# Optimization experiments

Hardware: AMD Instinct MI355X
Metric: run time of the kernel (lower is better)

## Reference

```python
import jax, jax.numpy as jnp
import numpy as np

N_NODES = 100000
N_EDGES = 6400000
F_IN = 128
F_OUT = 16


def setup_inputs() -> dict:
    key = jax.random.key(0)
    k1, k2, k3 = jax.random.split(key, 3)
    x = jax.random.normal(k1, (N_NODES, F_IN), dtype=jnp.float32)
    edge_index = jax.random.randint(k2, (2, N_EDGES), 0, N_NODES, dtype=jnp.int64)
    W = jax.random.normal(k3, (F_IN, F_OUT), dtype=jnp.float32) / np.sqrt(F_IN)
    b = jnp.zeros((F_OUT,), dtype=jnp.float32)
    return {"x": x, "edge_index": edge_index, "W": W, "b": b}


def reference(x, edge_index, W, b):
    # GCNConv (PyG defaults: add self-loops, symmetric normalization) -> tanh -> mean pool
    N = x.shape[0]
    loops = jnp.arange(N, dtype=edge_index.dtype)
    row = jnp.concatenate([edge_index[0], loops])  # source nodes
    col = jnp.concatenate([edge_index[1], loops])  # target nodes
    # degree of target nodes (edge weight 1.0)
    deg = jax.ops.segment_sum(jnp.ones(row.shape[0], dtype=x.dtype), col, num_segments=N)
    dinv = jnp.where(deg > 0, jax.lax.rsqrt(deg), 0.0)
    norm = dinv[row] * dinv[col]  # [E+N]
    h = x @ W  # [N, F_OUT] transform first (cheaper than transforming messages)
    msgs = h[row] * norm[:, None]  # gather + scale
    out = jax.ops.segment_sum(msgs, col, num_segments=N) + b  # scatter-add
    h = jnp.tanh(out)
    # MeanAggregation over all nodes -> single graph embedding [1, F_OUT]
    return jnp.mean(h, axis=0, keepdims=True)
```

## Files before the change

kernel.cpp:

```cpp
#include <hip/hip_runtime.h>
#include <math.h>

#define N_NODES 100000
#define N_EDGES 6400000
#define F_IN 128
#define F_OUT 16
#define NB 391
#define NBLK 1000
#define EPB 6400
#define BCAP 20480
#define KPB 5
#define QSCALE 1024.0f
#define QINV   (1.0f / 1024.0f)
#define FIN_GRID 640
#define GN 128
#define GSTRIDE 132

__global__ void __launch_bounds__(256) place_kernel(const int* __restrict__ row,
        const int* __restrict__ col, int* __restrict__ cur,
        unsigned int* __restrict__ packed) {
    __shared__ int hist[NB];
    __shared__ int scanb[512];
    __shared__ int base[NB];
    __shared__ int gadj[NB];
    __shared__ unsigned int tile[EPB];
    __shared__ unsigned char tileb8[EPB];
    const int t = threadIdx.x, k = blockIdx.x;
    const int e0 = k * EPB;
    for (int i = t; i < NB; i += 256) hist[i] = 0;
    __syncthreads();
    for (int i = t; i < EPB; i += 256)
        atomicAdd(&hist[col[e0 + i] >> 8], 1);
    __syncthreads();
    scanb[t] = (t < NB) ? hist[t] : 0;
    scanb[t + 256] = (t + 256 < NB) ? hist[t + 256] : 0;
    __syncthreads();
    for (int off = 1; off < 512; off <<= 1) {
        int a  = (t >= off) ? scanb[t - off] : 0;
        int a2 = scanb[t + 256 - off];
        __syncthreads();
        scanb[t] += a; scanb[t + 256] += a2;
        __syncthreads();
    }
    if (t < NB) base[t] = scanb[t] - hist[t];
    if (t + 256 < NB) base[t + 256] = scanb[t + 256] - hist[t + 256];
    __syncthreads();
    const int b256 = base[256];
    for (int bb = t; bb < NB; bb += 256) {
        int c = hist[bb];
        int g = (c > 0) ? atomicAdd(&cur[bb], c) : 0;
        gadj[bb] = bb * BCAP + g - base[bb];
        hist[bb] = 0;
    }
    __syncthreads();
    for (int i = t; i < EPB; i += 256) {
        int c = col[e0 + i];
        int r = row[e0 + i];
        int bb = c >> 8;
        int pos = base[bb] + atomicAdd(&hist[bb], 1);
        tile[pos] = ((unsigned)r << 8) | (unsigned)(c & 255);
        tileb8[pos] = (unsigned char)bb;
    }
    __syncthreads();
    for (int i = t; i < EPB; i += 256) {
        int bb = (int)tileb8[i] + ((i >= b256) ? 256 : 0);
        packed[gadj[bb] + i] = tile[i];
    }
}

__global__ void __launch_bounds__(256) deg_kernel(const unsigned int* __restrict__ packed,
        const int* __restrict__ cur, int* __restrict__ deg) {
    __shared__ int dh[256];
    const int t = threadIdx.x;
    dh[t] = 0;
    __syncthreads();
    const int b = blockIdx.x, part = blockIdx.y;
    const int cnt = cur[b];
    const int s = b * BCAP;
    const int chunk = (cnt + 3) >> 2;
    const int cs = s + part * chunk;
    const int ce = s + min((part + 1) * chunk, cnt);
    for (int i = cs + t; i < ce; i += 256)
        atomicAdd(&dh[packed[i] & 255u], 1);
    __syncthreads();
    const int node = (b << 8) + t;
    if (node < N_NODES && dh[t]) atomicAdd(&deg[node], dh[t]);
}

__global__ void __launch_bounds__(256) gemm_kernel(const float* __restrict__ x,
        const float* __restrict__ W, const int* __restrict__ deg,
        short* __restrict__ gq, int* __restrict__ acc) {
    __shared__ float Ws[F_IN * F_OUT];
    __shared__ float xs[GN * GSTRIDE];
    const int t = threadIdx.x;
    const int n0 = blockIdx.x * GN;
    {
        const size_t z0 = (size_t)blockIdx.x * 2048;
        for (int j = t; j < 2048; j += 256) {
            size_t idx = z0 + j;
            if (idx < (size_t)N_NODES * F_OUT) acc[idx] = 0;
        }
    }
    const float4* W4 = (const float4*)W;
    for (int i = t; i < 512; i += 256) ((float4*)Ws)[i] = W4[i];
    for (int i = t; i < GN * 32; i += 256) {
        int r = i >> 5, c4 = i & 31;
        float4 v = make_float4(0.f, 0.f, 0.f, 0.f);
        if (n0 + r < N_NODES)
            v = ((const float4*)(x + (size_t)(n0 + r) * F_IN))[c4];
        *(float4*)(xs + r * GSTRIDE + c4 * 4) = v;
    }
    __syncthreads();
    const int fq = t & 3, n2 = t >> 2;
    const float* xrA = xs + n2 * GSTRIDE;
    const float* xrB = xs + (n2 + 64) * GSTRIDE;
    float accA[4] = {0.f, 0.f, 0.f, 0.f};
    float accB[4] = {0.f, 0.f, 0.f, 0.f};
    #pragma unroll 8
    for (int kq = 0; kq < 32; kq++) {
        float4 xa = *(const float4*)(xrA + kq * 4);
        float4 xb = *(const float4*)(xrB + kq * 4);
        #pragma unroll
        for (int j = 0; j < 4; j++) {
            float4 w = *(const float4*)(Ws + (kq * 4 + j) * 16 + fq * 4);
            float a = (j == 0) ? xa.x : (j == 1) ? xa.y : (j == 2) ? xa.z : xa.w;
            float bv = (j == 0) ? xb.x : (j == 1) ? xb.y : (j == 2) ? xb.z : xb.w;
            accA[0] += a * w.x;  accA[1] += a * w.y;
            accA[2] += a * w.z;  accA[3] += a * w.w;
            accB[0] += bv * w.x; accB[1] += bv * w.y;
            accB[2] += bv * w.z; accB[3] += bv * w.w;
        }
    }
    const int gA = n0 + n2, gB = n0 + n2 + 64;
    if (gA < N_NODES) {
        float dinv = rsqrtf((float)deg[gA] + 1.0f);
        short4 o;
        float v0 = fminf(fmaxf(accA[0] * dinv * QSCALE, -32000.f), 32000.f);
        float v1 = fminf(fmaxf(accA[1] * dinv * QSCALE, -32000.f), 32000.f);
        float v2 = fminf(fmaxf(accA[2] * dinv * QSCALE, -32000.f), 32000.f);
        float v3 = fminf(fmaxf(accA[3] * dinv * QSCALE, -32000.f), 32000.f);
        o.x = (short)__float2int_rn(v0); o.y = (short)__float2int_rn(v1);
        o.z = (short)__float2int_rn(v2); o.w = (short)__float2int_rn(v3);
        *(short4*)(gq + (size_t)gA * 16 + fq * 4) = o;
    }
    if (gB < N_NODES) {
        float dinv = rsqrtf((float)deg[gB] + 1.0f);
        short4 o;
        float v0 = fminf(fmaxf(accB[0] * dinv * QSCALE, -32000.f), 32000.f);
        float v1 = fminf(fmaxf(accB[1] * dinv * QSCALE, -32000.f), 32000.f);
        float v2 = fminf(fmaxf(accB[2] * dinv * QSCALE, -32000.f), 32000.f);
        float v3 = fminf(fmaxf(accB[3] * dinv * QSCALE, -32000.f), 32000.f);
        o.x = (short)__float2int_rn(v0); o.y = (short)__float2int_rn(v1);
        o.z = (short)__float2int_rn(v2); o.w = (short)__float2int_rn(v3);
        *(short4*)(gq + (size_t)gB * 16 + fq * 4) = o;
    }
}

__global__ void __launch_bounds__(256) scatter_kernel(
        const unsigned int* __restrict__ packed, const int* __restrict__ cur,
        const short* __restrict__ gq, int* __restrict__ acc) {
    __shared__ int sacc[256 * F_OUT];
    const int t = threadIdx.x;
    for (int i = t; i < 256 * F_OUT; i += 256) sacc[i] = 0;
    __syncthreads();
    const int b = blockIdx.x, part = blockIdx.y;
    const int cnt = cur[b];
    const int s = b * BCAP;
    const int chunk = (cnt + KPB - 1) / KPB;
    const int cs = s + part * chunk;
    const int ce = s + min((part + 1) * chunk, cnt);
    const int f = t & 15, eg = t >> 4;
    int i = cs + eg;
    for (; i + 48 < ce; i += 64) {
        unsigned p0 = packed[i];
        unsigned p1 = packed[i + 16];
        unsigned p2 = packed[i + 32];
        unsigned p3 = packed[i + 48];
        int v0 = gq[(p0 >> 8) * 16 + f];
        int v1 = gq[(p1 >> 8) * 16 + f];
        int v2 = gq[(p2 >> 8) * 16 + f];
        int v3 = gq[(p3 >> 8) * 16 + f];
        atomicAdd(&sacc[((p0 & 255u) << 4) + f], v0);
        atomicAdd(&sacc[((p1 & 255u) << 4) + f], v1);
        atomicAdd(&sacc[((p2 & 255u) << 4) + f], v2);
        atomicAdd(&sacc[((p3 & 255u) << 4) + f], v3);
    }
    for (; i < ce; i += 16) {
        unsigned p0 = packed[i];
        atomicAdd(&sacc[((p0 & 255u) << 4) + f], (int)gq[(p0 >> 8) * 16 + f]);
    }
    __syncthreads();
    const int nbase = b << 8;
    for (int j = t; j < 256 * F_OUT; j += 256) {
        int v = sacc[j];
        if (v && nbase + (j >> 4) < N_NODES)
            atomicAdd(&acc[((size_t)nbase << 4) + j], v);
    }
}

__global__ void __launch_bounds__(256) finalize_kernel(const int* __restrict__ acc,
        const short* __restrict__ gq, const int* __restrict__ deg,
        const float* __restrict__ b, double* __restrict__ dsum,
        int* __restrict__ done, float* __restrict__ out) {
    __shared__ float s[4][16];
    __shared__ int lastflag;
    const int tid = threadIdx.x;
    const int f = tid & 15;
    const float bf = b[f];
    float local = 0.f;
    for (int i = blockIdx.x * blockDim.x + tid; i < N_NODES * F_OUT;
         i += gridDim.x * blockDim.x) {
        const int n = i >> 4;
        int ai = acc[i] + (int)gq[i];
        float dinvn = rsqrtf((float)deg[n] + 1.0f);
        local += tanhf(dinvn * ((float)ai * QINV) + bf);
    }
    local += __shfl_down(local, 32);
    local += __shfl_down(local, 16);
    const int lane = tid & 63, wave = tid >> 6;
    if (lane < 16) s[wave][lane] = local;
    __syncthreads();
    if (tid < 16) {
        float v = s[0][tid] + s[1][tid] + s[2][tid] + s[3][tid];
        atomicAdd(&dsum[tid], (double)v);
    }
    if (tid == 0) {
        __threadfence();
        lastflag = (atomicAdd(done, 1) == (int)gridDim.x - 1);
    }
    __syncthreads();
    if (lastflag && tid < 16) {
        double v = atomicAdd(&dsum[tid], 0.0);
        out[tid] = (float)(v * (1.0 / (double)N_NODES));
    }
}

extern "C" void kernel_launch(void* const* d_in, const int* in_sizes, int n_in,
                              void* d_out, int out_size, void* d_ws, size_t ws_size,
                              hipStream_t stream) {
    const float* x  = (const float*)d_in[0];
    const int*   ei = (const int*)d_in[1];
    const float* W  = (const float*)d_in[2];
    const float* b  = (const float*)d_in[3];
    float* out = (float*)d_out;

    const int* row = ei;
    const int* col = ei + N_EDGES;

    char* p = (char*)d_ws;
    double*       dsum   = (double*)p;        p += 128;
    int*          done   = (int*)p;           p += 32;
    int*          cur    = (int*)p;           p += 1600;
    int*          deg    = (int*)p;           p += (size_t)N_NODES * 4;
    int*          acc    = (int*)p;           p += (size_t)N_NODES * F_OUT * 4;
    short*        gq     = (short*)p;         p += (size_t)N_NODES * F_OUT * 2;
    unsigned int* packed = (unsigned int*)p;

    hipMemsetAsync(dsum, 0, 128 + 32 + 1600 + (size_t)N_NODES * 4, stream);

    place_kernel   <<<NBLK, 256, 0, stream>>>(row, col, cur, packed);
    deg_kernel     <<<dim3(NB, 4), 256, 0, stream>>>(packed, cur, deg);
    gemm_kernel    <<<(N_NODES + GN - 1) / GN, 256, 0, stream>>>(x, W, deg, gq, acc);
    scatter_kernel <<<dim3(NB, KPB), 256, 0, stream>>>(packed, cur, gq, acc);
    finalize_kernel<<<FIN_GRID, 256, 0, stream>>>(acc, gq, deg, b, dsum, done, out);
}
```

Before: 292.7 us.

## Fuse finalize into scatter via last-block-per-bucket, simplify GEMM to direct loads

Removes the separate finalize kernel. The last of the KPB scatter blocks for each 256-node bucket, detected with a per-bucket counter, computes tanh and the partial mean for that bucket, and a grid-level counter writes the output. The GEMM drops its shared-memory staging of x and reads rows straight from global memory, 64 nodes per block. KPB rises from 5 to 8 for more scatter parallelism. This saves a launch and a full pass over acc, at the cost of extra atomics and fences in the scatter tail.

```diff
diff --git a/kernel.cpp b/kernel.cpp
--- a/kernel.cpp
+++ b/kernel.cpp
@@ -9,12 +9,9 @@
 #define NBLK 1000
 #define EPB 6400
 #define BCAP 20480
-#define KPB 5
+#define KPB 8
 #define QSCALE 1024.0f
 #define QINV   (1.0f / 1024.0f)
-#define FIN_GRID 640
-#define GN 128
-#define GSTRIDE 132
 
 __global__ void __launch_bounds__(256) place_kernel(const int* __restrict__ row,
         const int* __restrict__ col, int* __restrict__ cur,
@@ -91,84 +88,64 @@
         const float* __restrict__ W, const int* __restrict__ deg,
         short* __restrict__ gq, int* __restrict__ acc) {
     __shared__ float Ws[F_IN * F_OUT];
-    __shared__ float xs[GN * GSTRIDE];
     const int t = threadIdx.x;
-    const int n0 = blockIdx.x * GN;
     {
-        const size_t z0 = (size_t)blockIdx.x * 2048;
-        for (int j = t; j < 2048; j += 256) {
+        const size_t z0 = (size_t)blockIdx.x * 1024;
+        for (int j = t; j < 1024; j += 256) {
             size_t idx = z0 + j;
             if (idx < (size_t)N_NODES * F_OUT) acc[idx] = 0;
         }
     }
     const float4* W4 = (const float4*)W;
     for (int i = t; i < 512; i += 256) ((float4*)Ws)[i] = W4[i];
-    for (int i = t; i < GN * 32; i += 256) {
-        int r = i >> 5, c4 = i & 31;
-        float4 v = make_float4(0.f, 0.f, 0.f, 0.f);
-        if (n0 + r < N_NODES)
-            v = ((const float4*)(x + (size_t)(n0 + r) * F_IN))[c4];
-        *(float4*)(xs + r * GSTRIDE + c4 * 4) = v;
-    }
-    __syncthreads();
-    const int fq = t & 3, n2 = t >> 2;
-    const float* xrA = xs + n2 * GSTRIDE;
-    const float* xrB = xs + (n2 + 64) * GSTRIDE;
-    float accA[4] = {0.f, 0.f, 0.f, 0.f};
-    float accB[4] = {0.f, 0.f, 0.f, 0.f};
-    #pragma unroll 8
+    __syncthreads();
+    const int fq = t & 3, n = t >> 2;
+    const int node = blockIdx.x * 64 + n;
+    if (node >= N_NODES) return;
+    const float4* xr = (const float4*)(x + (size_t)node * F_IN);
+    float a0 = 0.f, a1 = 0.f, a2 = 0.f, a3 = 0.f;
+    #pragma unroll 4
     for (int kq = 0; kq < 32; kq++) {
-        float4 xa = *(const float4*)(xrA + kq * 4);
-        float4 xb = *(const float4*)(xrB + kq * 4);
-        #pragma unroll
-        for (int j = 0; j < 4; j++) {
-            float4 w = *(const float4*)(Ws + (kq * 4 + j) * 16 + fq * 4);
-            float a = (j == 0) ? xa.x : (j == 1) ? xa.y : (j == 2) ? xa.z : xa.w;
-            float bv = (j == 0) ? xb.x : (j == 1) ? xb.y : (j == 2) ? xb.z : xb.w;
-            accA[0] += a * w.x;  accA[1] += a * w.y;
-            accA[2] += a * w.z;  accA[3] += a * w.w;
-            accB[0] += bv * w.x; accB[1] += bv * w.y;
-            accB[2] += bv * w.z; accB[3] += bv * w.w;
-        }
-    }
-    const int gA = n0 + n2, gB = n0 + n2 + 64;
-    if (gA < N_NODES) {
-        float dinv = rsqrtf((float)deg[gA] + 1.0f);
-        short4 o;
-        float v0 = fminf(fmaxf(accA[0] * dinv * QSCALE, -32000.f), 32000.f);
-        float v1 = fminf(fmaxf(accA[1] * dinv * QSCALE, -32000.f), 32000.f);
-        float v2 = fminf(fmaxf(accA[2] * dinv * QSCALE, -32000.f), 32000.f);
-        float v3 = fminf(fmaxf(accA[3] * dinv * QSCALE, -32000.f), 32000.f);
-        o.x = (short)__float2int_rn(v0); o.y = (short)__float2int_rn(v1);
-        o.z = (short)__float2int_rn(v2); o.w = (short)__float2int_rn(v3);
-        *(short4*)(gq + (size_t)gA * 16 + fq * 4) = o;
-    }
-    if (gB < N_NODES) {
-        float dinv = rsqrtf((float)deg[gB] + 1.0f);
-        short4 o;
-        float v0 = fminf(fmaxf(accB[0] * dinv * QSCALE, -32000.f), 32000.f);
-        float v1 = fminf(fmaxf(accB[1] * dinv * QSCALE, -32000.f), 32000.f);
-        float v2 = fminf(fmaxf(accB[2] * dinv * QSCALE, -32000.f), 32000.f);
-        float v3 = fminf(fmaxf(accB[3] * dinv * QSCALE, -32000.f), 32000.f);
-        o.x = (short)__float2int_rn(v0); o.y = (short)__float2int_rn(v1);
-        o.z = (short)__float2int_rn(v2); o.w = (short)__float2int_rn(v3);
-        *(short4*)(gq + (size_t)gB * 16 + fq * 4) = o;
-    }
+        float4 xa = xr[kq];
+        const float* wb = Ws + kq * 64 + fq * 4;
+        float4 w0 = *(const float4*)(wb);
+        float4 w1 = *(const float4*)(wb + 16);
+        float4 w2 = *(const float4*)(wb + 32);
+        float4 w3 = *(const float4*)(wb + 48);
+        a0 += xa.x * w0.x + xa.y * w1.x + xa.z * w2.x + xa.w * w3.x;
+        a1 += xa.x * w0.y + xa.y * w1.y + xa.z * w2.y + xa.w * w3.y;
+        a2 += xa.x * w0.z + xa.y * w1.z + xa.z * w2.z + xa.w * w3.z;
+        a3 += xa.x * w0.w + xa.y * w1.w + xa.z * w2.w + xa.w * w3.w;
+    }
+    const float dinv = rsqrtf((float)deg[node] + 1.0f);
+    short4 o;
+    float v0 = fminf(fmaxf(a0 * dinv * QSCALE, -32000.f), 32000.f);
+    float v1 = fminf(fmaxf(a1 * dinv * QSCALE, -32000.f), 32000.f);
+    float v2 = fminf(fmaxf(a2 * dinv * QSCALE, -32000.f), 32000.f);
+    float v3 = fminf(fmaxf(a3 * dinv * QSCALE, -32000.f), 32000.f);
+    o.x = (short)__float2int_rn(v0); o.y = (short)__float2int_rn(v1);
+    o.z = (short)__float2int_rn(v2); o.w = (short)__float2int_rn(v3);
+    *(short4*)(gq + (size_t)node * 16 + fq * 4) = o;
 }
 
 __global__ void __launch_bounds__(256) scatter_kernel(
         const unsigned int* __restrict__ packed, const int* __restrict__ cur,
-        const short* __restrict__ gq, int* __restrict__ acc) {
+        const short* __restrict__ gq, int* __restrict__ acc,
+        const int* __restrict__ deg, const float* __restrict__ bvec,
+        int* __restrict__ bdone, double* __restrict__ dsum,
+        int* __restrict__ done, float* __restrict__ out) {
     __shared__ int sacc[256 * F_OUT];
+    __shared__ float s[4][16];
+    __shared__ int lastflag, gridlast;
     const int t = threadIdx.x;
     for (int i = t; i < 256 * F_OUT; i += 256) sacc[i] = 0;
     __syncthreads();
     const int b = blockIdx.x, part = blockIdx.y;
     const int cnt = cur[b];
-    const int s = b * BCAP;
+    const int sbase = b * BCAP;
     const int chunk = (cnt + KPB - 1) / KPB;
-    const int cs = s + part * chunk;
-    const int ce = s + min((part + 1) * chunk, cnt);
+    const int cs = sbase + part * chunk;
+    const int ce = sbase + min((part + 1) * chunk, cnt);
     const int f = t & 15, eg = t >> 4;
     int i = cs + eg;
     for (; i + 48 < ce; i += 64) {
@@ -196,42 +173,40 @@
         if (v && nbase + (j >> 4) < N_NODES)
             atomicAdd(&acc[((size_t)nbase << 4) + j], v);
     }
-}
-
-__global__ void __launch_bounds__(256) finalize_kernel(const int* __restrict__ acc,
-        const short* __restrict__ gq, const int* __restrict__ deg,
-        const float* __restrict__ b, double* __restrict__ dsum,
-        int* __restrict__ done, float* __restrict__ out) {
-    __shared__ float s[4][16];
-    __shared__ int lastflag;
-    const int tid = threadIdx.x;
-    const int f = tid & 15;
-    const float bf = b[f];
+    __threadfence();
+    if (t == 0) lastflag = (atomicAdd(&bdone[b], 1) == KPB - 1);
+    __syncthreads();
+    if (!lastflag) return;
+    __threadfence();
+    const float bf = bvec[f];
     float local = 0.f;
-    for (int i = blockIdx.x * blockDim.x + tid; i < N_NODES * F_OUT;
-         i += gridDim.x * blockDim.x) {
-        const int n = i >> 4;
-        int ai = acc[i] + (int)gq[i];
-        float dinvn = rsqrtf((float)deg[n] + 1.0f);
-        local += tanhf(dinvn * ((float)ai * QINV) + bf);
+    for (int j = t; j < 256 * F_OUT; j += 256) {
+        const int nn = nbase + (j >> 4);
+        if (nn < N_NODES) {
+            int av = __hip_atomic_load(&acc[((size_t)nbase << 4) + j],
+                                       __ATOMIC_RELAXED, __HIP_MEMORY_SCOPE_AGENT);
+            int ai = av + (int)gq[((size_t)nbase << 4) + j];
+            float dinvn = rsqrtf((float)deg[nn] + 1.0f);
+            local += tanhf(dinvn * ((float)ai * QINV) + bf);
+        }
     }
     local += __shfl_down(local, 32);
     local += __shfl_down(local, 16);
-    const int lane = tid & 63, wave = tid >> 6;
+    const int lane = t & 63, wave = t >> 6;
     if (lane < 16) s[wave][lane] = local;
     __syncthreads();
-    if (tid < 16) {
-        float v = s[0][tid] + s[1][tid] + s[2][tid] + s[3][tid];
-        atomicAdd(&dsum[tid], (double)v);
-    }
-    if (tid == 0) {
+    if (t < 16) {
+        float v = s[0][t] + s[1][t] + s[2][t] + s[3][t];
+        atomicAdd(&dsum[t], (double)v);
+    }
+    if (t == 0) {
         __threadfence();
-        lastflag = (atomicAdd(done, 1) == (int)gridDim.x - 1);
-    }
-    __syncthreads();
-    if (lastflag && tid < 16) {
-        double v = atomicAdd(&dsum[tid], 0.0);
-        out[tid] = (float)(v * (1.0 / (double)N_NODES));
+        gridlast = (atomicAdd(done, 1) == NB - 1);
+    }
+    __syncthreads();
+    if (gridlast && t < 16) {
+        double v = atomicAdd(&dsum[t], 0.0);
+        out[t] = (float)(v * (1.0 / (double)N_NODES));
     }
 }
 
@@ -250,17 +225,18 @@
     char* p = (char*)d_ws;
     double*       dsum   = (double*)p;        p += 128;
     int*          done   = (int*)p;           p += 32;
+    int*          bdone  = (int*)p;           p += 1568;
     int*          cur    = (int*)p;           p += 1600;
     int*          deg    = (int*)p;           p += (size_t)N_NODES * 4;
     int*          acc    = (int*)p;           p += (size_t)N_NODES * F_OUT * 4;
     short*        gq     = (short*)p;         p += (size_t)N_NODES * F_OUT * 2;
     unsigned int* packed = (unsigned int*)p;
 
-    hipMemsetAsync(dsum, 0, 128 + 32 + 1600 + (size_t)N_NODES * 4, stream);
+    hipMemsetAsync(dsum, 0, 128 + 32 + 1568 + 1600 + (size_t)N_NODES * 4, stream);
 
     place_kernel   <<<NBLK, 256, 0, stream>>>(row, col, cur, packed);
     deg_kernel     <<<dim3(NB, 4), 256, 0, stream>>>(packed, cur, deg);
-    gemm_kernel    <<<(N_NODES + GN - 1) / GN, 256, 0, stream>>>(x, W, deg, gq, acc);
-    scatter_kernel <<<dim3(NB, KPB), 256, 0, stream>>>(packed, cur, gq, acc);
-    finalize_kernel<<<FIN_GRID, 256, 0, stream>>>(acc, gq, deg, b, dsum, done, out);
-}
+    gemm_kernel    <<<(N_NODES + 63) / 64, 256, 0, stream>>>(x, W, deg, gq, acc);
+    scatter_kernel <<<dim3(NB, KPB), 256, 0, stream>>>(packed, cur, gq, acc,
+                                                       deg, b, bdone, dsum, done, out);
+}
```

New measurement: 504.6 us. 72.4% more time.
